# Performance work log

Hardware: AMD Instinct MI355X
Metric: run time of the kernel (lower is better)

## Reference

```python
import jax, jax.numpy as jnp
import numpy as np

N_NODES = 100_000
N_EDGES = 1_600_000
F_IN = 128
N_CLASSES = 16
EPS = 1e-5


def setup_inputs() -> dict:
    key = jax.random.key(0)
    ks = jax.random.split(key, 32)

    def w(i, shape):
        # kaiming-ish small init
        fan_in = shape[0]
        return jax.random.normal(ks[i], shape, jnp.float32) * (1.0 / np.sqrt(fan_in))

    inp = {
        "x": jax.random.normal(ks[0], (N_NODES, F_IN), jnp.float32),
        "edge_index": jax.random.randint(ks[1], (2, N_EDGES), 0, N_NODES, dtype=jnp.int64),
        "edge_weight": jax.random.uniform(ks[2], (N_EDGES,), jnp.float32),
        # lin_in: 128 -> 64
        "lin_in_w": w(3, (F_IN, 64)), "lin_in_b": jnp.zeros((64,), jnp.float32),
        # conv1: 64 -> 128
        "conv1_w": w(4, (64, 128)), "conv1_b": jnp.zeros((128,), jnp.float32),
        "bn1_g": jnp.ones((128,), jnp.float32), "bn1_b": jnp.zeros((128,), jnp.float32),
        "bn1_m": jax.random.normal(ks[5], (128,), jnp.float32) * 0.1,
        "bn1_v": jax.random.uniform(ks[6], (128,), jnp.float32) + 0.5,
        # conv2: 128 -> 128
        "conv2_w": w(7, (128, 128)), "conv2_b": jnp.zeros((128,), jnp.float32),
        "bn2_g": jnp.ones((128,), jnp.float32), "bn2_b": jnp.zeros((128,), jnp.float32),
        "bn2_m": jax.random.normal(ks[8], (128,), jnp.float32) * 0.1,
        "bn2_v": jax.random.uniform(ks[9], (128,), jnp.float32) + 0.5,
        # conv3: 128 -> 64
        "conv3_w": w(10, (128, 64)), "conv3_b": jnp.zeros((64,), jnp.float32),
        "bn3_g": jnp.ones((64,), jnp.float32), "bn3_b": jnp.zeros((64,), jnp.float32),
        "bn3_m": jax.random.normal(ks[11], (64,), jnp.float32) * 0.1,
        "bn3_v": jax.random.uniform(ks[12], (64,), jnp.float32) + 0.5,
        # lin_out: 64 -> num_classes
        "lin_out_w": w(13, (64, N_CLASSES)), "lin_out_b": jnp.zeros((N_CLASSES,), jnp.float32),
    }
    return inp


def _gcn_forward(x, edge_index, edge_weight,
                 lin_in_w, lin_in_b,
                 conv1_w, conv1_b, bn1_g, bn1_b, bn1_m, bn1_v,
                 conv2_w, conv2_b, bn2_g, bn2_b, bn2_m, bn2_v,
                 conv3_w, conv3_b, bn3_g, bn3_b, bn3_m, bn3_v,
                 lin_out_w, lin_out_b):
    num_nodes = x.shape[0]
    src, dst = edge_index[0], edge_index[1]

    # PyG gcn_norm with self-loops (weight 1.0):
    # deg_i = 1 + sum_{j->i} w_ji ; norm_e = d_src^-1/2 * w_e * d_dst^-1/2
    deg = jax.ops.segment_sum(edge_weight, dst, num_segments=num_nodes) + 1.0
    dinv = jax.lax.rsqrt(deg)  # deg >= 1 always (self-loop)
    norm = dinv[src] * edge_weight * dinv[dst]       # [E]
    self_norm = dinv * dinv                           # [N], self-loop coeff

    def conv(h, w, b):
        h = h @ w                                     # [N, F_out]
        agg = jax.ops.segment_sum(h[src] * norm[:, None], dst,
                                  num_segments=num_nodes)
        return agg + h * self_norm[:, None] + b

    def bn(h, g, b, m, v):  # eval-mode batchnorm (running stats)
        return (h - m) * jax.lax.rsqrt(v + EPS) * g + b

    h = jax.nn.relu(x @ lin_in_w + lin_in_b)
    h = jax.nn.relu(bn(conv(h, conv1_w, conv1_b), bn1_g, bn1_b, bn1_m, bn1_v))
    # dropout p=0.3 is identity in eval mode
    h = jax.nn.relu(bn(conv(h, conv2_w, conv2_b), bn2_g, bn2_b, bn2_m, bn2_v))
    h = jax.nn.relu(bn(conv(h, conv3_w, conv3_b), bn3_g, bn3_b, bn3_m, bn3_v))
    return jax.nn.log_softmax(h @ lin_out_w + lin_out_b, axis=1)


def reference(x, edge_index, edge_weight,
              lin_in_w, lin_in_b,
              conv1_w, conv1_b, bn1_g, bn1_b, bn1_m, bn1_v,
              conv2_w, conv2_b, bn2_g, bn2_b, bn2_m, bn2_v,
              conv3_w, conv3_b, bn3_g, bn3_b, bn3_m, bn3_v,
              lin_out_w, lin_out_b):
    return _gcn_forward(x, edge_index, edge_weight,
                        lin_in_w, lin_in_b,
                        conv1_w, conv1_b, bn1_g, bn1_b, bn1_m, bn1_v,
                        conv2_w, conv2_b, bn2_g, bn2_b, bn2_m, bn2_v,
                        conv3_w, conv3_b, bn3_g, bn3_b, bn3_m, bn3_v,
                        lin_out_w, lin_out_b)
```

## Files before the change

kernel.cpp:

```cpp
#include <hip/hip_runtime.h>
#include <cstddef>
#include <cstdint>

#define EPSV 1e-5f

typedef unsigned int uint;
typedef unsigned short ushort;
typedef unsigned char uchar;
typedef short s16x8 __attribute__((ext_vector_type(8)));
typedef float f32x4 __attribute__((ext_vector_type(4)));

static __device__ __forceinline__ ushort f2bf(float f) {
    uint u = __float_as_uint(f);
    u = (u + 0x7fffu + ((u >> 16) & 1u)) >> 16;
    return (ushort)u;
}
static __device__ __forceinline__ float bf2f(ushort h) {
    return __uint_as_float(((uint)h) << 16);
}
static __device__ __forceinline__ uchar f2fp8(float v) {
    float f = v * 0x1p-120f;
    uint u = __float_as_uint(f);
    uint r = (u & 0x7fffffffu) + 0x7ffffu + ((u >> 20) & 1u);
    return (uchar)(((u >> 24) & 0x80u) | ((r >> 20) & 0x7fu));
}

#define NRM_SCALE 32768.0f
#define CAP 64
#define NRANGE 8
#define FILL_CHUNKS 512

__global__ __launch_bounds__(256) void k_prep_wt(const float* __restrict__ w0,
                                                 const float* __restrict__ w1,
                                                 const float* __restrict__ w2,
                                                 const float* __restrict__ w3,
                                                 ushort* __restrict__ wt0,
                                                 ushort* __restrict__ wt1,
                                                 ushort* __restrict__ wt2,
                                                 ushort* __restrict__ wt3) {
    int i = blockIdx.x * 256 + threadIdx.x;
    if (i < 8192) {
        int k = i >> 6, c = i & 63;
        wt0[c * 128 + k] = f2bf(w0[i]);
    } else if (i < 16384) {
        int j = i - 8192;
        int k = j >> 7, c = j & 127;
        wt1[c * 64 + k] = f2bf(w1[j]);
    } else if (i < 32768) {
        int j = i - 16384;
        int k = j >> 7, c = j & 127;
        wt2[c * 128 + k] = f2bf(w2[j]);
    } else if (i < 40960) {
        int j = i - 32768;
        int k = j >> 6, c = j & 63;
        wt3[c * 128 + k] = f2bf(w3[j]);
    }
}

template <int FIN, int FOUT, int EP, bool XF32, bool OUT8, bool SCALER>
__device__ __forceinline__ void gemm_body(int bid, const void* __restrict__ Xv,
                                          const ushort* __restrict__ WT,
                                          const float* __restrict__ bias,
                                          const float* __restrict__ bng,
                                          const float* __restrict__ bnb,
                                          const float* __restrict__ bnm,
                                          const float* __restrict__ bnv,
                                          const float* __restrict__ dinv,
                                          void* __restrict__ Yv, int n) {
    constexpr int LDW = FIN + 8;
    constexpr int NT = FOUT / 16;
    constexpr int KS = FIN / 32;
    __shared__ ushort sWT[FOUT * LDW];

    const int tid = threadIdx.x;
    const uint4* WT16 = (const uint4*)WT;
    for (int i = tid; i < FOUT * (FIN / 8); i += 256) {
        int row = i / (FIN / 8), c = i % (FIN / 8);
        ((uint4*)(sWT + row * LDW))[c] = WT16[i];
    }
    __syncthreads();

    const int wave = tid >> 6, lane = tid & 63;
    const int lrow = lane & 15, h = lane >> 4;
    const int node0 = bid * 128 + wave * 32;
    int r0 = node0 + lrow, r1 = r0 + 16;
    int cr0 = (r0 < n) ? r0 : (n - 1);
    int cr1 = (r1 < n) ? r1 : (n - 1);

    f32x4 acc[2][NT];
#pragma unroll
    for (int nh = 0; nh < 2; ++nh)
#pragma unroll
        for (int t = 0; t < NT; ++t) acc[nh][t] = (f32x4){0.f, 0.f, 0.f, 0.f};

#pragma unroll
    for (int s = 0; s < KS; ++s) {
        s16x8 a0, a1;
        if (XF32) {
            const float* X = (const float*)Xv;
            const float4* p0 = (const float4*)(X + (size_t)cr0 * FIN + h * 8 + s * 32);
            const float4* p1 = (const float4*)(X + (size_t)cr1 * FIN + h * 8 + s * 32);
            float4 f0 = p0[0], f1 = p0[1];
            uint4 u;
            u.x = (uint)f2bf(f0.x) | ((uint)f2bf(f0.y) << 16);
            u.y = (uint)f2bf(f0.z) | ((uint)f2bf(f0.w) << 16);
            u.z = (uint)f2bf(f1.x) | ((uint)f2bf(f1.y) << 16);
            u.w = (uint)f2bf(f1.z) | ((uint)f2bf(f1.w) << 16);
            a0 = *(s16x8*)&u;
            float4 g0 = p1[0], g1 = p1[1];
            uint4 v;
            v.x = (uint)f2bf(g0.x) | ((uint)f2bf(g0.y) << 16);
            v.y = (uint)f2bf(g0.z) | ((uint)f2bf(g0.w) << 16);
            v.z = (uint)f2bf(g1.x) | ((uint)f2bf(g1.y) << 16);
            v.w = (uint)f2bf(g1.z) | ((uint)f2bf(g1.w) << 16);
            a1 = *(s16x8*)&v;
        } else {
            const ushort* Xb = (const ushort*)Xv;
            uint4 u = *(const uint4*)(Xb + (size_t)cr0 * FIN + h * 8 + s * 32);
            uint4 v = *(const uint4*)(Xb + (size_t)cr1 * FIN + h * 8 + s * 32);
            a0 = *(s16x8*)&u;
            a1 = *(s16x8*)&v;
        }
#pragma unroll
        for (int t = 0; t < NT; ++t) {
            uint4 bw = *(const uint4*)(sWT + (t * 16 + lrow) * LDW + h * 8 + s * 32);
            s16x8 b = *(s16x8*)&bw;
            acc[0][t] = __builtin_amdgcn_mfma_f32_16x16x32_bf16(a0, b, acc[0][t], 0, 0, 0);
            acc[1][t] = __builtin_amdgcn_mfma_f32_16x16x32_bf16(a1, b, acc[1][t], 0, 0, 0);
        }
    }

    float sc[NT], of[NT];
#pragma unroll
    for (int t = 0; t < NT; ++t) {
        int c = t * 16 + lrow;
        if (EP == 1) {
            sc[t] = 1.f; of[t] = bias[c];
        } else if (EP == 2) {
            float s_ = rsqrtf(bnv[c] + EPSV) * bng[c];
            sc[t] = s_;
            of[t] = (bias[c] - bnm[c]) * s_ + bnb[c];
        } else {
            sc[t] = 1.f; of[t] = 0.f;
        }
    }
#pragma unroll
    for (int nh = 0; nh < 2; ++nh) {
#pragma unroll
        for (int r = 0; r < 4; ++r) {
            int row = node0 + nh * 16 + h * 4 + r;
            if (row < n) {
                float rs = SCALER ? dinv[row] : 1.f;
#pragma unroll
                for (int t = 0; t < NT; ++t) {
                    float y = acc[nh][t][r] * sc[t] + of[t];
                    if (EP >= 1) y = fmaxf(y, 0.f);
                    y *= rs;
                    if (OUT8)
                        ((uchar*)Yv)[(size_t)row * FOUT + t * 16 + lrow] = f2fp8(y);
                    else
                        ((ushort*)Yv)[(size_t)row * FOUT + t * 16 + lrow] = f2bf(y);
                }
            }
        }
    }
}

template <int FIN, int FOUT, int EP, bool XF32, bool OUT8, bool SCALER>
__global__ __launch_bounds__(256) void k_gemm_mfma(const void* __restrict__ Xv,
                                                   const ushort* __restrict__ WT,
                                                   const float* __restrict__ bias,
                                                   const float* __restrict__ bng,
                                                   const float* __restrict__ bnb,
                                                   const float* __restrict__ bnm,
                                                   const float* __restrict__ bnv,
                                                   const float* __restrict__ dinv,
                                                   void* __restrict__ Yv, int n) {
    gemm_body<FIN, FOUT, EP, XF32, OUT8, SCALER>(blockIdx.x, Xv, WT, bias, bng, bnb, bnm,
                                                 bnv, dinv, Yv, n);
}

__global__ __launch_bounds__(256) void k_fill_lin(const int* __restrict__ src,
                                                  const int* __restrict__ dst,
                                                  const float* __restrict__ ew,
                                                  int* __restrict__ cursor,
                                                  uint* __restrict__ csr, int e,
                                                  int nFill, int nNodes,
                                                  const float* __restrict__ x,
                                                  const ushort* __restrict__ wt0,
                                                  const float* __restrict__ lin_b,
                                                  ushort* __restrict__ B1, int n) {
    int bid = blockIdx.x;
    if (bid < nFill) {
        const int range = bid & (NRANGE - 1);
        const int chunk = bid >> 3;
        const int lo = (int)(((long long)range * nNodes) / NRANGE);
        const int hi = (int)(((long long)(range + 1) * nNodes) / NRANGE);
        const int e4 = e >> 2;
        const int4* dst4 = (const int4*)dst;
        for (int j = chunk * 256 + (int)threadIdx.x; j < e4; j += FILL_CHUNKS * 256) {
            int4 d4 = dst4[j];
            int base = j * 4;
#pragma unroll
            for (int k = 0; k < 4; ++k) {
                int d = (k == 0) ? d4.x : (k == 1) ? d4.y : (k == 2) ? d4.z : d4.w;
                if (d >= lo && d < hi) {
                    int i = base + k;
                    int s = src[i];
                    float w = ew[i];
                    uint wq = (uint)(w * NRM_SCALE + 0.5f);
                    wq = (wq > 32767u) ? 32767u : wq;
                    int slot = atomicAdd(&cursor[d], 1);
                    if (slot < CAP) csr[(size_t)d * CAP + slot] = ((uint)s << 15) | wq;
                }
            }
        }
        if (range == 0 && chunk == 0 && (int)threadIdx.x < (e & 3)) {
            int i = (e4 << 2) + (int)threadIdx.x;
            int d = dst[i];
            if (d >= lo && d < hi) {
            }
        }
    } else {
        gemm_body<128, 64, 1, true, false, false>(bid - nFill, x, wt0, lin_b,
                                                  nullptr, nullptr, nullptr, nullptr,
                                                  nullptr, B1, n);
    }
}

__global__ __launch_bounds__(64) void k_fill_tail(const int* __restrict__ src,
                                                  const int* __restrict__ dst,
                                                  const float* __restrict__ ew,
                                                  int* __restrict__ cursor,
                                                  uint* __restrict__ csr, int e) {
    int t = threadIdx.x;
    int e4 = e >> 2;
    int i = (e4 << 2) + t;
    if (i < e) {
        int s = src[i], d = dst[i];
        uint wq = (uint)(ew[i] * NRM_SCALE + 0.5f);
        wq = (wq > 32767u) ? 32767u : wq;
        int slot = atomicAdd(&cursor[d], 1);
        if (slot < CAP) csr[(size_t)d * CAP + slot] = ((uint)s << 15) | wq;
    }
}

__global__ __launch_bounds__(256) void k_deg_scale(const uint* __restrict__ csr,
                                                   const int* __restrict__ cursor,
                                                   const ushort* __restrict__ B1,
                                                   float* __restrict__ dinv,
                                                   uchar* __restrict__ B8, int n) {
    const int lane = threadIdx.x & 7;
    const int grp = threadIdx.x >> 3;
    const int node = blockIdx.x * 32 + grp;
    if (node >= n) return;
    int c = cursor[node];
    c = (c > CAP) ? CAP : c;
    uint s = 0;
    for (int j = lane; j < c; j += 8) s += csr[(size_t)node * CAP + j] & 0x7fffu;
    float fs = (float)s;
#pragma unroll
    for (int off = 4; off >= 1; off >>= 1) fs += __shfl_xor(fs, off, 8);
    float dd = rsqrtf(1.0f + fs * (1.0f / NRM_SCALE));
    if (lane == 0) dinv[node] = dd;

    uint4 u = ((const uint4*)B1)[(size_t)node * 8 + lane];
    uchar b[8];
    b[0] = f2fp8(__uint_as_float(u.x << 16) * dd);
    b[1] = f2fp8(__uint_as_float(u.x & 0xffff0000u) * dd);
    b[2] = f2fp8(__uint_as_float(u.y << 16) * dd);
    b[3] = f2fp8(__uint_as_float(u.y & 0xffff0000u) * dd);
    b[4] = f2fp8(__uint_as_float(u.z << 16) * dd);
    b[5] = f2fp8(__uint_as_float(u.z & 0xffff0000u) * dd);
    b[6] = f2fp8(__uint_as_float(u.w << 16) * dd);
    b[7] = f2fp8(__uint_as_float(u.w & 0xffff0000u) * dd);
    uint2 w;
    w.x = (uint)b[0] | ((uint)b[1] << 8) | ((uint)b[2] << 16) | ((uint)b[3] << 24);
    w.y = (uint)b[4] | ((uint)b[5] << 8) | ((uint)b[6] << 16) | ((uint)b[7] << 24);
    ((uint2*)B8)[(size_t)node * 8 + lane] = w;
}

#define DEC4(A, w, o, nvs)                                                         \
    {                                                                              \
        uint b0 = (w) & 0xffu, b1 = ((w) >> 8) & 0xffu;                            \
        uint b2 = ((w) >> 16) & 0xffu, b3 = (w) >> 24;                             \
        A[o]     = fmaf(__uint_as_float(((b0 & 0x80u) << 24) | ((b0 & 0x7fu) << 20)), nvs, A[o]);     \
        A[o + 1] = fmaf(__uint_as_float(((b1 & 0x80u) << 24) | ((b1 & 0x7fu) << 20)), nvs, A[o + 1]); \
        A[o + 2] = fmaf(__uint_as_float(((b2 & 0x80u) << 24) | ((b2 & 0x7fu) << 20)), nvs, A[o + 2]); \
        A[o + 3] = fmaf(__uint_as_float(((b3 & 0x80u) << 24) | ((b3 & 0x7fu) << 20)), nvs, A[o + 3]); \
    }

template <int FOUT, bool POST>
__global__ __launch_bounds__(256) void k_agg_fp8(const int* __restrict__ cursor,
                                                 const uint* __restrict__ csr,
                                                 const uchar* __restrict__ H8,
                                                 const float* __restrict__ dinv,
                                                 const float* __restrict__ cb,
                                                 const float* __restrict__ g,
                                                 const float* __restrict__ bb,
                                                 const float* __restrict__ m,
                                                 const float* __restrict__ v,
                                                 ushort* __restrict__ OUT, int n) {
    constexpr int TPG = FOUT / 8;
    constexpr int GPB = 256 / TPG;
    const int lane = threadIdx.x % TPG;
    const int grp = threadIdx.x / TPG;
    const int node = blockIdx.x * GPB + grp;
    if (node >= n) return;

    int c = cursor[node];
    c = (c > CAP) ? CAP : c;
    const int e0 = node * CAP, e1 = node * CAP + c;
    const uint2* H2 = (const uint2*)H8;
    const int ld = FOUT / 8;

    float acca[8], accb[8];
#pragma unroll
    for (int i = 0; i < 8; ++i) { acca[i] = 0.f; accb[i] = 0.f; }

    int e = e0;
    for (; e + 2 <= e1; e += 2) {
        uint p0 = csr[e], p1 = csr[e + 1];
        uint2 q0 = H2[(size_t)(p0 >> 15) * ld + lane];
        uint2 q1 = H2[(size_t)(p1 >> 15) * ld + lane];
        float n0 = (float)(p0 & 0x7fffu) * (0x1p+105f);
        float n1 = (float)(p1 & 0x7fffu) * (0x1p+105f);
        DEC4(acca, q0.x, 0, n0) DEC4(acca, q0.y, 4, n0)
        DEC4(accb, q1.x, 0, n1) DEC4(accb, q1.y, 4, n1)
    }
    if (e < e1) {
        uint p0 = csr[e];
        uint2 q0 = H2[(size_t)(p0 >> 15) * ld + lane];
        float n0 = (float)(p0 & 0x7fffu) * (0x1p+105f);
        DEC4(acca, q0.x, 0, n0) DEC4(acca, q0.y, 4, n0)
    }
    {
        uint2 q = H2[(size_t)node * ld + lane];
        DEC4(accb, q.x, 0, 0x1p+120f) DEC4(accb, q.y, 4, 0x1p+120f)
    }

    const float dd = dinv[node];
    float o[8];
    if (POST) {
        float4 cb0 = ((const float4*)cb)[lane * 2], cb1 = ((const float4*)cb)[lane * 2 + 1];
        float4 m0 = ((const float4*)m)[lane * 2], m1 = ((const float4*)m)[lane * 2 + 1];
        float4 v0 = ((const float4*)v)[lane * 2], v1 = ((const float4*)v)[lane * 2 + 1];
        float4 g0 = ((const float4*)g)[lane * 2], g1 = ((const float4*)g)[lane * 2 + 1];
        float4 b0 = ((const float4*)bb)[lane * 2], b1 = ((const float4*)bb)[lane * 2 + 1];
        o[0] = fmaxf(((acca[0] + accb[0]) * dd + cb0.x - m0.x) * rsqrtf(v0.x + EPSV) * g0.x + b0.x, 0.f);
        o[1] = fmaxf(((acca[1] + accb[1]) * dd + cb0.y - m0.y) * rsqrtf(v0.y + EPSV) * g0.y + b0.y, 0.f);
        o[2] = fmaxf(((acca[2] + accb[2]) * dd + cb0.z - m0.z) * rsqrtf(v0.z + EPSV) * g0.z + b0.z, 0.f);
        o[3] = fmaxf(((acca[3] + accb[3]) * dd + cb0.w - m0.w) * rsqrtf(v0.w + EPSV) * g0.w + b0.w, 0.f);
        o[4] = fmaxf(((acca[4] + accb[4]) * dd + cb1.x - m1.x) * rsqrtf(v1.x + EPSV) * g1.x + b1.x, 0.f);
        o[5] = fmaxf(((acca[5] + accb[5]) * dd + cb1.y - m1.y) * rsqrtf(v1.y + EPSV) * g1.y + b1.y, 0.f);
        o[6] = fmaxf(((acca[6] + accb[6]) * dd + cb1.z - m1.z) * rsqrtf(v1.z + EPSV) * g1.z + b1.z, 0.f);
        o[7] = fmaxf(((acca[7] + accb[7]) * dd + cb1.w - m1.w) * rsqrtf(v1.w + EPSV) * g1.w + b1.w, 0.f);
    } else {
#pragma unroll
        for (int i = 0; i < 8; ++i) o[i] = (acca[i] + accb[i]) * dd;
    }
    uint4 w;
    w.x = (uint)f2bf(o[0]) | ((uint)f2bf(o[1]) << 16);
    w.y = (uint)f2bf(o[2]) | ((uint)f2bf(o[3]) << 16);
    w.z = (uint)f2bf(o[4]) | ((uint)f2bf(o[5]) << 16);
    w.w = (uint)f2bf(o[6]) | ((uint)f2bf(o[7]) << 16);
    ((uint4*)OUT)[(size_t)node * (FOUT / 8) + lane] = w;
}

__global__ __launch_bounds__(256) void k_agg3_out(const int* __restrict__ cursor,
                                                  const uint* __restrict__ csr,
                                                  const uchar* __restrict__ H8,
                                                  const float* __restrict__ dinv,
                                                  const float* __restrict__ cb,
                                                  const float* __restrict__ g,
                                                  const float* __restrict__ bb,
                                                  const float* __restrict__ m,
                                                  const float* __restrict__ v,
                                                  const float* __restrict__ W,
                                                  const float* __restrict__ bias,
                                                  float* __restrict__ OUT, int n) {
    __shared__ float sW[64 * 16];
    __shared__ float sB[16];
    __shared__ float sH[32][64];

    const int tid = threadIdx.x;
    for (int i = tid; i < 64 * 16; i += 256) sW[i] = W[i];
    if (tid < 16) sB[tid] = bias[tid];

    const int lane = tid & 7;
    const int grp = tid >> 3;
    const int node = blockIdx.x * 32 + grp;
    const int nodeC = (node < n) ? node : (n - 1);
    const bool valid = node < n;

    int c = cursor[nodeC];
    c = (c > CAP) ? CAP : c;
    const int e0 = nodeC * CAP, e1 = nodeC * CAP + c;
    const uint2* H2 = (const uint2*)H8;

    float acca[8], accb[8];
#pragma unroll
    for (int i = 0; i < 8; ++i) { acca[i] = 0.f; accb[i] = 0.f; }

    int e = e0;
    for (; e + 2 <= e1; e += 2) {
        uint p0 = csr[e], p1 = csr[e + 1];
        uint2 q0 = H2[(size_t)(p0 >> 15) * 8 + lane];
        uint2 q1 = H2[(size_t)(p1 >> 15) * 8 + lane];
        float n0 = (float)(p0 & 0x7fffu) * (0x1p+105f);
        float n1 = (float)(p1 & 0x7fffu) * (0x1p+105f);
        DEC4(acca, q0.x, 0, n0) DEC4(acca, q0.y, 4, n0)
        DEC4(accb, q1.x, 0, n1) DEC4(accb, q1.y, 4, n1)
    }
    if (e < e1) {
        uint p0 = csr[e];
        uint2 q0 = H2[(size_t)(p0 >> 15) * 8 + lane];
        float n0 = (float)(p0 & 0x7fffu) * (0x1p+105f);
        DEC4(acca, q0.x, 0, n0) DEC4(acca, q0.y, 4, n0)
    }
    {
        uint2 q = H2[(size_t)nodeC * 8 + lane];
        DEC4(accb, q.x, 0, 0x1p+120f) DEC4(accb, q.y, 4, 0x1p+120f)
    }

    const float dd = dinv[nodeC];
    float4 cb0 = ((const float4*)cb)[lane * 2], cb1 = ((const float4*)cb)[lane * 2 + 1];
    float4 m0 = ((const float4*)m)[lane * 2], m1 = ((const float4*)m)[lane * 2 + 1];
    float4 v0 = ((const float4*)v)[lane * 2], v1 = ((const float4*)v)[lane * 2 + 1];
    float4 g0 = ((const float4*)g)[lane * 2], g1 = ((const float4*)g)[lane * 2 + 1];
    float4 b0 = ((const float4*)bb)[lane * 2], b1 = ((const float4*)bb)[lane * 2 + 1];
    float o[8];
    o[0] = fmaxf(((acca[0] + accb[0]) * dd + cb0.x - m0.x) * rsqrtf(v0.x + EPSV) * g0.x + b0.x, 0.f);
    o[1] = fmaxf(((acca[1] + accb[1]) * dd + cb0.y - m0.y) * rsqrtf(v0.y + EPSV) * g0.y + b0.y, 0.f);
    o[2] = fmaxf(((acca[2] + accb[2]) * dd + cb0.z - m0.z) * rsqrtf(v0.z + EPSV) * g0.z + b0.z, 0.f);
    o[3] = fmaxf(((acca[3] + accb[3]) * dd + cb0.w - m0.w) * rsqrtf(v0.w + EPSV) * g0.w + b0.w, 0.f);
    o[4] = fmaxf(((acca[4] + accb[4]) * dd + cb1.x - m1.x) * rsqrtf(v1.x + EPSV) * g1.x + b1.x, 0.f);
    o[5] = fmaxf(((acca[5] + accb[5]) * dd + cb1.y - m1.y) * rsqrtf(v1.y + EPSV) * g1.y + b1.y, 0.f);
    o[6] = fmaxf(((acca[6] + accb[6]) * dd + cb1.z - m1.z) * rsqrtf(v1.z + EPSV) * g1.z + b1.z, 0.f);
    o[7] = fmaxf(((acca[7] + accb[7]) * dd + cb1.w - m1.w) * rsqrtf(v1.w + EPSV) * g1.w + b1.w, 0.f);

#pragma unroll
    for (int i = 0; i < 8; ++i) sH[grp][lane * 8 + i] = o[i];
    __syncthreads();

    const int c0 = lane * 2;
    float y0 = sB[c0], y1 = sB[c0 + 1];
#pragma unroll
    for (int k = 0; k < 64; ++k) {
        float hk = sH[grp][k];
        y0 = fmaf(hk, sW[k * 16 + c0], y0);
        y1 = fmaf(hk, sW[k * 16 + c0 + 1], y1);
    }

    float mx = fmaxf(y0, y1);
#pragma unroll
    for (int off = 4; off >= 1; off >>= 1) mx = fmaxf(mx, __shfl_xor(mx, off, 8));
    float s = expf(y0 - mx) + expf(y1 - mx);
#pragma unroll
    for (int off = 4; off >= 1; off >>= 1) s += __shfl_xor(s, off, 8);
    float ls = logf(s);

    if (valid) {
        float2 out2 = make_float2(y0 - mx - ls, y1 - mx - ls);
        *(float2*)(OUT + (size_t)node * 16 + c0) = out2;
    }
}

extern "C" void kernel_launch(void* const* d_in, const int* in_sizes, int n_in,
                              void* d_out, int out_size, void* d_ws, size_t ws_size,
                              hipStream_t stream) {
    const float* x        = (const float*)d_in[0];
    const int*   ei       = (const int*)d_in[1];
    const float* ew       = (const float*)d_in[2];
    const float* lin_in_w = (const float*)d_in[3];
    const float* lin_in_b = (const float*)d_in[4];
    const float* c1w = (const float*)d_in[5];
    const float* c1b = (const float*)d_in[6];
    const float* bn1g = (const float*)d_in[7];
    const float* bn1b = (const float*)d_in[8];
    const float* bn1m = (const float*)d_in[9];
    const float* bn1v = (const float*)d_in[10];
    const float* c2w = (const float*)d_in[11];
    const float* c2b = (const float*)d_in[12];
    const float* bn2g = (const float*)d_in[13];
    const float* bn2b = (const float*)d_in[14];
    const float* bn2m = (const float*)d_in[15];
    const float* bn2v = (const float*)d_in[16];
    const float* c3w = (const float*)d_in[17];
    const float* c3b = (const float*)d_in[18];
    const float* bn3g = (const float*)d_in[19];
    const float* bn3b = (const float*)d_in[20];
    const float* bn3m = (const float*)d_in[21];
    const float* bn3v = (const float*)d_in[22];
    const float* low = (const float*)d_in[23];
    const float* lob = (const float*)d_in[24];

    const int N = in_sizes[0] / 128;
    const int E = in_sizes[2];
    const int* src = ei;
    const int* dst = ei + E;

    char* p = (char*)d_ws;
    auto alloc = [&](size_t bytes) {
        char* r = p;
        p += (bytes + 15) & ~(size_t)15;
        return (void*)r;
    };
    float* dinv  = (float*)alloc((size_t)N * 4);
    int* cursor  = (int*)alloc((size_t)N * 4);
    uint* csr    = (uint*)alloc((size_t)N * CAP * 4);
    ushort* B1   = (ushort*)alloc((size_t)N * 128 * 2);
    ushort* B2   = (ushort*)alloc((size_t)N * 128 * 2);
    uchar* B8    = (uchar*)alloc((size_t)N * 128);
    ushort* wt0  = (ushort*)alloc(8192 * 2);
    ushort* wt1  = (ushort*)alloc(8192 * 2);
    ushort* wt2  = (ushort*)alloc(16384 * 2);
    ushort* wt3  = (ushort*)alloc(8192 * 2);
    if ((size_t)(p - (char*)d_ws) > ws_size) return;

    auto cdiv = [](int a, int b) { return (a + b - 1) / b; };
    const int nFill = NRANGE * FILL_CHUNKS;

    k_prep_wt<<<160, 256, 0, stream>>>(lin_in_w, c1w, c2w, c3w, wt0, wt1, wt2, wt3);
    hipMemsetAsync(cursor, 0, (size_t)N * 4, stream);

    k_fill_lin<<<nFill + cdiv(N, 128), 256, 0, stream>>>(
        src, dst, ew, cursor, csr, E, nFill, N, x, wt0, lin_in_b, B1, N);
    if (E & 3) k_fill_tail<<<1, 64, 0, stream>>>(src, dst, ew, cursor, csr, E);

    k_deg_scale<<<cdiv(N, 32), 256, 0, stream>>>(csr, cursor, B1, dinv, B8, N);

    k_agg_fp8<64, false><<<cdiv(N, 32), 256, 0, stream>>>(cursor, csr, B8, dinv,
                                                          nullptr, nullptr, nullptr, nullptr,
                                                          nullptr, B2, N);
    k_gemm_mfma<64, 128, 2, false, false, false><<<cdiv(N, 128), 256, 0, stream>>>(
        B2, wt1, c1b, bn1g, bn1b, bn1m, bn1v, nullptr, B1, N);

    k_gemm_mfma<128, 128, 0, false, true, true><<<cdiv(N, 128), 256, 0, stream>>>(
        B1, wt2, nullptr, nullptr, nullptr, nullptr, nullptr, dinv, B8, N);
    k_agg_fp8<128, true><<<cdiv(N, 16), 256, 0, stream>>>(cursor, csr, B8, dinv,
                                                          c2b, bn2g, bn2b, bn2m, bn2v, B2, N);

    k_gemm_mfma<128, 64, 0, false, true, true><<<cdiv(N, 128), 256, 0, stream>>>(
        B2, wt3, nullptr, nullptr, nullptr, nullptr, nullptr, dinv, B8, N);
    k_agg3_out<<<cdiv(N, 32), 256, 0, stream>>>(cursor, csr, B8, dinv,
                                                c3b, bn3g, bn3b, bn3m, bn3v,
                                                low, lob, (float*)d_out, N);
}
```

Measured before the change: 266.7 us.

## Replace range-filtered CSR fill with two-pass bucketed partition by destination range

The old fill kernel had each of 8 destination ranges rescan all edges and atomically insert matching ones. It is replaced by a one-pass partition kernel that stages edges per range in shared memory, then flushes them to global sub-buckets, with an overflow list for edges that do not fit. A second kernel drains each bucket into the capped CSR using per-node atomics. This removes the 8x redundant reads of dst, src and weights, at the cost of an extra kernel launch, an intermediate bucket buffer write and read, and serial overflow handling.

```diff
diff --git a/kernel.cpp b/kernel.cpp
--- a/kernel.cpp
+++ b/kernel.cpp
@@ -28,7 +28,11 @@
 #define NRM_SCALE 32768.0f
 #define CAP 64
 #define NRANGE 8
-#define FILL_CHUNKS 512
+#define NSUB 128
+#define CAPSUB 2560
+#define STAGE 320
+#define OVF_CAP 65536
+#define PA_BLOCKS 1024
 
 __global__ __launch_bounds__(256) void k_prep_wt(const float* __restrict__ w0,
                                                  const float* __restrict__ w1,
@@ -180,68 +184,129 @@
                                                  bnv, dinv, Yv, n);
 }
 
-__global__ __launch_bounds__(256) void k_fill_lin(const int* __restrict__ src,
-                                                  const int* __restrict__ dst,
-                                                  const float* __restrict__ ew,
-                                                  int* __restrict__ cursor,
-                                                  uint* __restrict__ csr, int e,
-                                                  int nFill, int nNodes,
-                                                  const float* __restrict__ x,
-                                                  const ushort* __restrict__ wt0,
-                                                  const float* __restrict__ lin_b,
-                                                  ushort* __restrict__ B1, int n) {
+__global__ __launch_bounds__(256) void k_bucket_lin(const int* __restrict__ src,
+                                                    const int* __restrict__ dst,
+                                                    const float* __restrict__ ew,
+                                                    int e, int nNodes,
+                                                    uint* __restrict__ gcur,
+                                                    uint2* __restrict__ bucket,
+                                                    uint* __restrict__ ovfcnt,
+                                                    uint2* __restrict__ ovf,
+                                                    const float* __restrict__ x,
+                                                    const ushort* __restrict__ wt0,
+                                                    const float* __restrict__ lin_b,
+                                                    ushort* __restrict__ B1, int n) {
     int bid = blockIdx.x;
-    if (bid < nFill) {
-        const int range = bid & (NRANGE - 1);
-        const int chunk = bid >> 3;
-        const int lo = (int)(((long long)range * nNodes) / NRANGE);
-        const int hi = (int)(((long long)(range + 1) * nNodes) / NRANGE);
-        const int e4 = e >> 2;
-        const int4* dst4 = (const int4*)dst;
-        for (int j = chunk * 256 + (int)threadIdx.x; j < e4; j += FILL_CHUNKS * 256) {
+    if (bid >= PA_BLOCKS) {
+        gemm_body<128, 64, 1, true, false, false>(bid - PA_BLOCKS, x, wt0, lin_b,
+                                                  nullptr, nullptr, nullptr, nullptr,
+                                                  nullptr, B1, n);
+        return;
+    }
+    __shared__ uint scnt[NRANGE];
+    __shared__ uint sbase[NRANGE];
+    __shared__ uint2 sbuf[NRANGE][STAGE];
+
+    const int tid = threadIdx.x;
+    const int sub = bid & (NSUB - 1);
+    const int e4 = e >> 2;
+    const int rs = (nNodes + NRANGE - 1) / NRANGE;
+    const int iters = (e4 + PA_BLOCKS * 256 - 1) / (PA_BLOCKS * 256);
+    const int4* dst4 = (const int4*)dst;
+
+    for (int it = 0; it < iters; ++it) {
+        if (tid < NRANGE) scnt[tid] = 0;
+        __syncthreads();
+
+        int j = (it * PA_BLOCKS + bid) * 256 + tid;
+        if (j < e4) {
             int4 d4 = dst4[j];
             int base = j * 4;
 #pragma unroll
             for (int k = 0; k < 4; ++k) {
                 int d = (k == 0) ? d4.x : (k == 1) ? d4.y : (k == 2) ? d4.z : d4.w;
-                if (d >= lo && d < hi) {
-                    int i = base + k;
-                    int s = src[i];
-                    float w = ew[i];
-                    uint wq = (uint)(w * NRM_SCALE + 0.5f);
-                    wq = (wq > 32767u) ? 32767u : wq;
-                    int slot = atomicAdd(&cursor[d], 1);
-                    if (slot < CAP) csr[(size_t)d * CAP + slot] = ((uint)s << 15) | wq;
+                int i = base + k;
+                int s = src[i];
+                float w = ew[i];
+                uint wq = (uint)(w * NRM_SCALE + 0.5f);
+                wq = (wq > 32767u) ? 32767u : wq;
+                uint pk = ((uint)s << 15) | wq;
+                int r = d / rs;
+                uint pos = atomicAdd(&scnt[r], 1u);
+                if (pos < STAGE) {
+                    sbuf[r][pos] = make_uint2(pk, (uint)d);
+                } else {
+                    uint op = atomicAdd(ovfcnt, 1u);
+                    if (op < OVF_CAP) ovf[op] = make_uint2(pk, (uint)d);
                 }
             }
         }
-        if (range == 0 && chunk == 0 && (int)threadIdx.x < (e & 3)) {
-            int i = (e4 << 2) + (int)threadIdx.x;
-            int d = dst[i];
-            if (d >= lo && d < hi) {
+        __syncthreads();
+
+        if (tid < NRANGE) {
+            uint c = scnt[tid];
+            c = (c > STAGE) ? STAGE : c;
+            scnt[tid] = c;
+            sbase[tid] = atomicAdd(&gcur[tid * NSUB + sub], c);
+        }
+        __syncthreads();
+
+        for (int r = 0; r < NRANGE; ++r) {
+            uint c = scnt[r], b = sbase[r];
+            for (uint p2 = tid; p2 < c; p2 += 256) {
+                uint gp = b + p2;
+                uint2 v = sbuf[r][p2];
+                if (gp < CAPSUB)
+                    bucket[((size_t)r * NSUB + sub) * CAPSUB + gp] = v;
+                else {
+                    uint op = atomicAdd(ovfcnt, 1u);
+                    if (op < OVF_CAP) ovf[op] = v;
+                }
             }
         }
-    } else {
-        gemm_body<128, 64, 1, true, false, false>(bid - nFill, x, wt0, lin_b,
-                                                  nullptr, nullptr, nullptr, nullptr,
-                                                  nullptr, B1, n);
-    }
-}
-
-__global__ __launch_bounds__(64) void k_fill_tail(const int* __restrict__ src,
-                                                  const int* __restrict__ dst,
-                                                  const float* __restrict__ ew,
-                                                  int* __restrict__ cursor,
-                                                  uint* __restrict__ csr, int e) {
-    int t = threadIdx.x;
-    int e4 = e >> 2;
-    int i = (e4 << 2) + t;
-    if (i < e) {
+        __syncthreads();
+    }
+
+    if (bid == 0 && tid < (e & 3)) {
+        int i = (e4 << 2) + tid;
         int s = src[i], d = dst[i];
         uint wq = (uint)(ew[i] * NRM_SCALE + 0.5f);
         wq = (wq > 32767u) ? 32767u : wq;
+        uint op = atomicAdd(ovfcnt, 1u);
+        if (op < OVF_CAP) ovf[op] = make_uint2(((uint)s << 15) | wq, (uint)d);
+    }
+}
+
+__global__ __launch_bounds__(256) void k_fillcsr_b(const uint* __restrict__ gcur,
+                                                   const uint2* __restrict__ bucket,
+                                                   const uint* __restrict__ ovfcnt,
+                                                   const uint2* __restrict__ ovf,
+                                                   int* __restrict__ cursor,
+                                                   uint* __restrict__ csr, int nNodes) {
+    const int bid = blockIdx.x;
+    const int r = bid & (NRANGE - 1);
+    const int sub = bid >> 3;
+    uint cnt = gcur[r * NSUB + sub];
+    cnt = (cnt > CAPSUB) ? CAPSUB : cnt;
+    const uint2* bk = bucket + ((size_t)r * NSUB + sub) * CAPSUB;
+    for (uint i = threadIdx.x; i < cnt; i += 256) {
+        uint2 v = bk[i];
+        int d = (int)v.y;
         int slot = atomicAdd(&cursor[d], 1);
-        if (slot < CAP) csr[(size_t)d * CAP + slot] = ((uint)s << 15) | wq;
+        if (slot < CAP) csr[(size_t)d * CAP + slot] = v.x;
+    }
+    if (sub == 0) {
+        const int rs = (nNodes + NRANGE - 1) / NRANGE;
+        uint oc = *ovfcnt;
+        oc = (oc > OVF_CAP) ? OVF_CAP : oc;
+        for (uint i = threadIdx.x; i < oc; i += 256) {
+            uint2 v = ovf[i];
+            int d = (int)v.y;
+            if (d / rs == r) {
+                int slot = atomicAdd(&cursor[d], 1);
+                if (slot < CAP) csr[(size_t)d * CAP + slot] = v.x;
+            }
+        }
     }
 }
 
@@ -506,27 +571,31 @@
         p += (bytes + 15) & ~(size_t)15;
         return (void*)r;
     };
-    float* dinv  = (float*)alloc((size_t)N * 4);
-    int* cursor  = (int*)alloc((size_t)N * 4);
-    uint* csr    = (uint*)alloc((size_t)N * CAP * 4);
-    ushort* B1   = (ushort*)alloc((size_t)N * 128 * 2);
-    ushort* B2   = (ushort*)alloc((size_t)N * 128 * 2);
-    uchar* B8    = (uchar*)alloc((size_t)N * 128);
-    ushort* wt0  = (ushort*)alloc(8192 * 2);
-    ushort* wt1  = (ushort*)alloc(8192 * 2);
-    ushort* wt2  = (ushort*)alloc(16384 * 2);
-    ushort* wt3  = (ushort*)alloc(8192 * 2);
+    float* dinv   = (float*)alloc((size_t)N * 4);
+    int* cursor   = (int*)alloc(((size_t)N + NRANGE * NSUB + 4) * 4);
+    uint* gcur    = (uint*)(cursor + N);
+    uint* ovfcnt  = (uint*)(gcur + NRANGE * NSUB);
+    uint* csr     = (uint*)alloc((size_t)N * CAP * 4);
+    uint2* bucket = (uint2*)alloc((size_t)NRANGE * NSUB * CAPSUB * 8);
+    uint2* ovf    = (uint2*)alloc((size_t)OVF_CAP * 8);
+    ushort* B1    = (ushort*)alloc((size_t)N * 128 * 2);
+    ushort* B2    = (ushort*)alloc((size_t)N * 128 * 2);
+    uchar* B8     = (uchar*)alloc((size_t)N * 128);
+    ushort* wt0   = (ushort*)alloc(8192 * 2);
+    ushort* wt1   = (ushort*)alloc(8192 * 2);
+    ushort* wt2   = (ushort*)alloc(16384 * 2);
+    ushort* wt3   = (ushort*)alloc(8192 * 2);
     if ((size_t)(p - (char*)d_ws) > ws_size) return;
 
     auto cdiv = [](int a, int b) { return (a + b - 1) / b; };
-    const int nFill = NRANGE * FILL_CHUNKS;
 
     k_prep_wt<<<160, 256, 0, stream>>>(lin_in_w, c1w, c2w, c3w, wt0, wt1, wt2, wt3);
-    hipMemsetAsync(cursor, 0, (size_t)N * 4, stream);
-
-    k_fill_lin<<<nFill + cdiv(N, 128), 256, 0, stream>>>(
-        src, dst, ew, cursor, csr, E, nFill, N, x, wt0, lin_in_b, B1, N);
-    if (E & 3) k_fill_tail<<<1, 64, 0, stream>>>(src, dst, ew, cursor, csr, E);
+    hipMemsetAsync(cursor, 0, ((size_t)N + NRANGE * NSUB + 4) * 4, stream);
+
+    k_bucket_lin<<<PA_BLOCKS + cdiv(N, 128), 256, 0, stream>>>(
+        src, dst, ew, E, N, gcur, bucket, ovfcnt, ovf, x, wt0, lin_in_b, B1, N);
+
+    k_fillcsr_b<<<NRANGE * NSUB, 256, 0, stream>>>(gcur, bucket, ovfcnt, ovf, cursor, csr, N);
 
     k_deg_scale<<<cdiv(N, 32), 256, 0, stream>>>(csr, cursor, B1, dinv, B8, N);
 
```

Measured after the change: 299.9 us. +12.4%, slower.
